# Kernel optimization log

Hardware: AMD Instinct MI355X
Metric: run time of the kernel (lower is better)

The kernel has to match this reference:

```python
import jax, jax.numpy as jnp
import numpy as np

HIDDEN = 2048
N_HEADS = 32
N_KV = 8
HEAD_DIM = HIDDEN // N_HEADS  # 64
GROUP = N_HEADS // N_KV       # 4
FFN = 8192
EPS = 1e-5
ROPE_BASE = 500000.0
NEG = -1e9


def rms_norm(x, w, eps=EPS):
    var = jnp.mean(x * x, axis=-1, keepdims=True)
    return x * jax.lax.rsqrt(var + eps) * w


def rope_cos_sin(position_ids):
    # inv_freq: [head_dim//2]
    inv_freq = 1.0 / (ROPE_BASE ** (jnp.arange(0, HEAD_DIM, 2, dtype=jnp.float32) / HEAD_DIM))
    freqs = position_ids.astype(jnp.float32)[:, :, None] * inv_freq[None, None, :]  # [b,s,d/2]
    emb = jnp.concatenate([freqs, freqs], axis=-1)  # [b,s,d]
    return jnp.cos(emb), jnp.sin(emb)


def rotate_half(x):
    x1, x2 = jnp.split(x, 2, axis=-1)
    return jnp.concatenate([-x2, x1], axis=-1)


def setup_inputs() -> dict:
    key = jax.random.key(0)
    ks = jax.random.split(key, 12)
    b, s = 2, 1024
    scale_h = 1.0 / np.sqrt(HIDDEN)
    scale_f = 1.0 / np.sqrt(FFN)
    hidden_states = jax.random.normal(ks[0], (b, s, HIDDEN), jnp.float32)
    causal = jnp.where(jnp.tril(jnp.ones((s, s), bool)), 0.0, NEG).astype(jnp.float32)
    attention_mask = jnp.broadcast_to(causal[None, None], (b, 1, s, s))
    position_ids = jnp.broadcast_to(jnp.arange(s, dtype=jnp.int32)[None], (b, s))
    return {
        "hidden_states": hidden_states,
        "attention_mask": attention_mask,
        "wq": jax.random.normal(ks[1], (HIDDEN, N_HEADS * HEAD_DIM), jnp.float32) * scale_h,
        "wk": jax.random.normal(ks[2], (HIDDEN, N_KV * HEAD_DIM), jnp.float32) * scale_h,
        "wv": jax.random.normal(ks[3], (HIDDEN, N_KV * HEAD_DIM), jnp.float32) * scale_h,
        "wo": jax.random.normal(ks[4], (N_HEADS * HEAD_DIM, HIDDEN), jnp.float32) * scale_h,
        "norm1_w": jnp.ones((HIDDEN,), jnp.float32),
        "norm2_w": jnp.ones((HIDDEN,), jnp.float32),
        "w_gate": jax.random.normal(ks[5], (HIDDEN, FFN), jnp.float32) * scale_h,
        "w_up": jax.random.normal(ks[6], (HIDDEN, FFN), jnp.float32) * scale_h,
        "w_down": jax.random.normal(ks[7], (FFN, HIDDEN), jnp.float32) * scale_f,
        "position_ids": position_ids,
    }


def reference(hidden_states, attention_mask, wq, wk, wv, wo, norm1_w, norm2_w,
              w_gate, w_up, w_down, position_ids):
    b, s, _ = hidden_states.shape
    residual = hidden_states
    normed = rms_norm(hidden_states, norm1_w)

    q = (normed @ wq).reshape(b, s, N_HEADS, HEAD_DIM).transpose(0, 2, 1, 3)  # [b,H,s,d]
    k = (normed @ wk).reshape(b, s, N_KV, HEAD_DIM).transpose(0, 2, 1, 3)    # [b,G,s,d]
    v = (normed @ wv).reshape(b, s, N_KV, HEAD_DIM).transpose(0, 2, 1, 3)

    cos, sin = rope_cos_sin(position_ids)  # [b,s,d]
    cos, sin = cos[:, None], sin[:, None]  # unsqueeze head dim
    q = q * cos + rotate_half(q) * sin
    k = k * cos + rotate_half(k) * sin

    # repeat_kv: [b,G,s,d] -> [b,H,s,d]
    k = jnp.repeat(k, GROUP, axis=1)
    v = jnp.repeat(v, GROUP, axis=1)

    scores = jnp.einsum('bhqd,bhkd->bhqk', q, k)
    scores = scores + attention_mask  # mask added BEFORE scaling, as in source
    attn = jax.nn.softmax(scores / np.sqrt(HEAD_DIM), axis=-1)
    ctx = jnp.einsum('bhqk,bhkd->bhqd', attn, v)
    ctx = ctx.transpose(0, 2, 1, 3).reshape(b, s, N_HEADS * HEAD_DIM)
    attn_out = ctx @ wo

    normed_ff = rms_norm(attn_out + residual, norm2_w)
    ff = (jax.nn.silu(normed_ff @ w_gate) * (normed_ff @ w_up)) @ w_down
    return attn_out + ff
```

## Files before the change

### kernel.cpp

```cpp
#include <hip/hip_runtime.h>
#include <hip/hip_bf16.h>
#include <cstddef>
#include <cstdint>

#define T_TOK   2048
#define HID     2048
#define NHEADS  32
#define NKV     8
#define HDIM    64
#define FFN_DIM 8192
#define QKV_N   3072

typedef __hip_bfloat16 bf16;
typedef __attribute__((ext_vector_type(8))) short short8;
typedef __attribute__((ext_vector_type(4))) float f32x4;
typedef __attribute__((ext_vector_type(4))) unsigned short us4;

typedef __attribute__((address_space(1))) const void cg_void;
typedef __attribute__((address_space(3))) void lds_void;

__global__ __launch_bounds__(256) void cast_transpose(const float* __restrict__ in,
                                                      bf16* __restrict__ out,
                                                      int K, int N)
{
    __shared__ bf16 t[64][65];
    const int n0 = blockIdx.x * 64, k0 = blockIdx.y * 64;
    const int tn = threadIdx.x & 63, tk = threadIdx.x >> 6;
    #pragma unroll
    for (int kk = tk; kk < 64; kk += 4)
        t[kk][tn] = __float2bfloat16(in[(size_t)(k0 + kk) * N + n0 + tn]);
    __syncthreads();
    #pragma unroll
    for (int nn = tk; nn < 64; nn += 4)
        out[(size_t)(n0 + nn) * K + k0 + tn] = t[tn][nn];
}

__global__ __launch_bounds__(256) void cast_ilv(const float* __restrict__ in,
                                                bf16* __restrict__ out,
                                                int N, int is_up)
{
    __shared__ bf16 t[64][65];
    const int n0 = blockIdx.x * 64, k0 = blockIdx.y * 64;
    const int tn = threadIdx.x & 63, tk = threadIdx.x >> 6;
    #pragma unroll
    for (int kk = tk; kk < 64; kk += 4)
        t[kk][tn] = __float2bfloat16(in[(size_t)(k0 + kk) * N + n0 + tn]);
    __syncthreads();
    #pragma unroll
    for (int nn = tk; nn < 64; nn += 4) {
        int n = n0 + nn;
        int r = ((n >> 5) << 6) + (is_up << 5) + (n & 31);
        out[(size_t)r * HID + k0 + tn] = t[tn][nn];
    }
}

__global__ __launch_bounds__(256) void rmsnorm_kernel(const float* __restrict__ x,
                                                      const float* __restrict__ w,
                                                      bf16* __restrict__ out)
{
    __shared__ float sm[4];
    const int row = blockIdx.x, tid = threadIdx.x;
    const float4* xr = (const float4*)(x + (size_t)row * HID);
    float4 a = xr[tid], b = xr[tid + 256];
    float ss = a.x*a.x + a.y*a.y + a.z*a.z + a.w*a.w
             + b.x*b.x + b.y*b.y + b.z*b.z + b.w*b.w;
    #pragma unroll
    for (int off = 32; off; off >>= 1) ss += __shfl_down(ss, off);
    if ((tid & 63) == 0) sm[tid >> 6] = ss;
    __syncthreads();
    float sc = rsqrtf((sm[0] + sm[1] + sm[2] + sm[3]) * (1.0f / HID) + 1e-5f);
    const float4* wr = (const float4*)w;
    float4 w0 = wr[tid], w1 = wr[tid + 256];
    bf16* o = out + (size_t)row * HID;
    o[tid*4+0] = __float2bfloat16(a.x * sc * w0.x);
    o[tid*4+1] = __float2bfloat16(a.y * sc * w0.y);
    o[tid*4+2] = __float2bfloat16(a.z * sc * w0.z);
    o[tid*4+3] = __float2bfloat16(a.w * sc * w0.w);
    o[1024+tid*4+0] = __float2bfloat16(b.x * sc * w1.x);
    o[1024+tid*4+1] = __float2bfloat16(b.y * sc * w1.y);
    o[1024+tid*4+2] = __float2bfloat16(b.z * sc * w1.z);
    o[1024+tid*4+3] = __float2bfloat16(b.w * sc * w1.w);
}

__global__ __launch_bounds__(256) void rmsnorm_add_kernel(const float* __restrict__ xa,
                                                          const float* __restrict__ xb,
                                                          const float* __restrict__ w,
                                                          bf16* __restrict__ out)
{
    __shared__ float sm[4];
    const int row = blockIdx.x, tid = threadIdx.x;
    const float4* ar = (const float4*)(xa + (size_t)row * HID);
    const float4* br = (const float4*)(xb + (size_t)row * HID);
    float4 a0 = ar[tid], a1 = ar[tid + 256];
    float4 b0 = br[tid], b1 = br[tid + 256];
    float4 s0, s1;
    s0.x = a0.x + b0.x; s0.y = a0.y + b0.y; s0.z = a0.z + b0.z; s0.w = a0.w + b0.w;
    s1.x = a1.x + b1.x; s1.y = a1.y + b1.y; s1.z = a1.z + b1.z; s1.w = a1.w + b1.w;
    float ss = s0.x*s0.x + s0.y*s0.y + s0.z*s0.z + s0.w*s0.w
             + s1.x*s1.x + s1.y*s1.y + s1.z*s1.z + s1.w*s1.w;
    #pragma unroll
    for (int off = 32; off; off >>= 1) ss += __shfl_down(ss, off);
    if ((tid & 63) == 0) sm[tid >> 6] = ss;
    __syncthreads();
    float sc = rsqrtf((sm[0] + sm[1] + sm[2] + sm[3]) * (1.0f / HID) + 1e-5f);
    const float4* wr = (const float4*)w;
    float4 w0 = wr[tid], w1 = wr[tid + 256];
    bf16* o = out + (size_t)row * HID;
    o[tid*4+0] = __float2bfloat16(s0.x * sc * w0.x);
    o[tid*4+1] = __float2bfloat16(s0.y * sc * w0.y);
    o[tid*4+2] = __float2bfloat16(s0.z * sc * w0.z);
    o[tid*4+3] = __float2bfloat16(s0.w * sc * w0.w);
    o[1024+tid*4+0] = __float2bfloat16(s1.x * sc * w1.x);
    o[1024+tid*4+1] = __float2bfloat16(s1.y * sc * w1.y);
    o[1024+tid*4+2] = __float2bfloat16(s1.z * sc * w1.z);
    o[1024+tid*4+3] = __float2bfloat16(s1.w * sc * w1.w);
}

template<int BN, int EPI>
__device__ __forceinline__ void gemm_body(
    const bf16* __restrict__ A, const bf16* __restrict__ Bt,
    float* __restrict__ Cf, bf16* __restrict__ Cb,
    int lda, int kbeg, int klen, int ldc, int bx, int by)
{
    constexpr int NFR = BN / 32;
    constexpr int BCH = BN / 32;
    __shared__ bf16 As[128 * 64];
    __shared__ bf16 Bs[BN * 64];
    const int tid = threadIdx.x;
    const int wv = tid >> 6, ln = tid & 63;
    const int wr = wv >> 1, wc = wv & 1;
    const size_t m0 = (size_t)by * 128;
    const size_t n0 = (size_t)bx * BN;

    const int lrow = ln >> 3;
    const int lk   = (ln & 7) ^ lrow;

    f32x4 acc[4][NFR] = {};

    const bf16* Abase = A  + (m0 + (size_t)wv*32 + lrow) * lda + kbeg + lk*8;
    const bf16* Bbase = Bt + (n0 + (size_t)wv*BCH*8 + lrow) * lda + kbeg + lk*8;
    bf16* AsW = As + wv*4*512;
    bf16* BsW = Bs + wv*BCH*512;

    for (int kt = 0; kt < klen; kt += 64) {
        #pragma unroll
        for (int i = 0; i < 4; ++i)
            __builtin_amdgcn_global_load_lds((cg_void*)(Abase + (size_t)i*8*lda + kt),
                                             (lds_void*)(AsW + i*512), 16, 0, 0);
        #pragma unroll
        for (int i = 0; i < BCH; ++i)
            __builtin_amdgcn_global_load_lds((cg_void*)(Bbase + (size_t)i*8*lda + kt),
                                             (lds_void*)(BsW + i*512), 16, 0, 0);
        __syncthreads();
        #pragma unroll
        for (int ks = 0; ks < 2; ++ks) {
            short8 af[4], bfg[NFR];
            const int kbyte = ks*64 + (ln >> 4)*16;
            #pragma unroll
            for (int m = 0; m < 4; ++m) {
                int row = wr*64 + m*16 + (ln & 15);
                af[m] = *(const short8*)((const char*)As + row*128 + (kbyte ^ ((row & 7) << 4)));
            }
            #pragma unroll
            for (int n = 0; n < NFR; ++n) {
                int row = wc*(BN/2) + n*16 + (ln & 15);
                bfg[n] = *(const short8*)((const char*)Bs + row*128 + (kbyte ^ ((row & 7) << 4)));
            }
            #pragma unroll
            for (int m = 0; m < 4; ++m)
                #pragma unroll
                for (int n = 0; n < NFR; ++n)
                    acc[m][n] = __builtin_amdgcn_mfma_f32_16x16x32_bf16(af[m], bfg[n], acc[m][n], 0, 0, 0);
        }
        __syncthreads();
    }

    const int cj = ln & 15, rj = ln >> 4;
    if constexpr (EPI == 4) {
        #pragma unroll
        for (int m = 0; m < 4; ++m) {
            #pragma unroll
            for (int j = 0; j < 4; ++j) {
                size_t row = m0 + wr*64 + m*16 + rj*4 + j;
                #pragma unroll
                for (int n = 0; n < 2; ++n) {
                    int col = ((int)(n0 >> 6) + wc) * 32 + n*16 + cj;
                    float g = acc[m][n][j];
                    float u = acc[m][n+2][j];
                    Cb[row * (size_t)ldc + col] =
                        __float2bfloat16(g / (1.0f + __expf(-g)) * u);
                }
            }
        }
    } else {
        #pragma unroll
        for (int m = 0; m < 4; ++m) {
            #pragma unroll
            for (int j = 0; j < 4; ++j) {
                size_t row = m0 + wr*64 + m*16 + rj*4 + j;
                #pragma unroll
                for (int n = 0; n < NFR; ++n) {
                    int col = (int)n0 + wc*(BN/2) + n*16 + cj;
                    float v = acc[m][n][j];
                    size_t off = row * (size_t)ldc + col;
                    if constexpr (EPI == 0) Cf[off] = v;
                    else if constexpr (EPI == 5) unsafeAtomicAdd(&Cf[off], v);
                }
            }
        }
    }
}

__device__ __forceinline__ void swz(int& bx, int& by) {
    const int nwg = gridDim.x * gridDim.y;
    int orig = blockIdx.y * gridDim.x + blockIdx.x;
    int wg = (orig & 7) * (nwg >> 3) + (orig >> 3);
    by = wg % gridDim.y;
    bx = wg / gridDim.y;
}

__global__ __launch_bounds__(256) void g_qkv(const bf16* __restrict__ A,
                                             const bf16* __restrict__ Bt,
                                             float* __restrict__ C) {
    int bx, by; swz(bx, by);
    gemm_body<64,0>(A, Bt, C, nullptr, HID, 0, HID, QKV_N, bx, by);
}
__global__ __launch_bounds__(256) void g_wo(const bf16* __restrict__ A,
                                            const bf16* __restrict__ Bt,
                                            float* __restrict__ C) {
    int bx, by; swz(bx, by);
    gemm_body<64,0>(A, Bt, C, nullptr, HID, 0, HID, HID, bx, by);
}
__global__ __launch_bounds__(256) void g_gateup(const bf16* __restrict__ A,
                                                const bf16* __restrict__ Bt,
                                                bf16* __restrict__ C) {
    int bx, by; swz(bx, by);
    gemm_body<128,4>(A, Bt, nullptr, C, HID, 0, HID, FFN_DIM, bx, by);
}
__global__ __launch_bounds__(256) void g_down(const bf16* __restrict__ A,
                                              const bf16* __restrict__ Bt,
                                              float* __restrict__ C) {
    int bx, by; swz(bx, by);
    gemm_body<64,5>(A, Bt, C, nullptr, FFN_DIM, blockIdx.z * 4096, 4096, HID, bx, by);
}

__global__ __launch_bounds__(256) void rope_cast(const float* __restrict__ qkv,
                                                 const int* __restrict__ pos_ids,
                                                 bf16* __restrict__ Qp,
                                                 bf16* __restrict__ Kp)
{
    const int t = blockIdx.x, tid = threadIdx.x;
    const int b = t >> 10, s = t & 1023;
    const float pos = (float)pos_ids[t];
    const float* row = qkv + (size_t)t * QKV_N;

    {
        int idx = tid * 4;
        int hq = idx >> 5, j = idx & 31;
        float xa[4], xb[4];
        *(float4*)xa = *(const float4*)(row + hq*64 + j);
        *(float4*)xb = *(const float4*)(row + hq*64 + j + 32);
        us4 o1, o2;
        #pragma unroll
        for (int jj = 0; jj < 4; ++jj) {
            float inv = exp2f(-(float)(j + jj) * 0.5916115177913804f);
            float ang = pos * inv, c, sn;
            sincosf(ang, &sn, &c);
            o1[jj] = __bfloat16_as_ushort(__float2bfloat16(xa[jj]*c - xb[jj]*sn));
            o2[jj] = __bfloat16_as_ushort(__float2bfloat16(xb[jj]*c + xa[jj]*sn));
        }
        bf16* qd = Qp + ((size_t)(b*32 + hq)*1024 + s)*64;
        *(us4*)(qd + j)      = o1;
        *(us4*)(qd + j + 32) = o2;
    }
    {
        int hk = tid >> 5, j = tid & 31;
        float a = row[2048 + hk*64 + j];
        float bb = row[2048 + hk*64 + j + 32];
        float inv = exp2f(-(float)j * 0.5916115177913804f);
        float ang = pos * inv, c, sn;
        sincosf(ang, &sn, &c);
        bf16* kd = Kp + ((size_t)(b*8 + hk)*1024 + s)*64;
        kd[j]      = __float2bfloat16(a*c - bb*sn);
        kd[j + 32] = __float2bfloat16(bb*c + a*sn);
    }
}

__global__ __launch_bounds__(256) void vt_cast(const float* __restrict__ qkv,
                                               bf16* __restrict__ Vt)
{
    __shared__ bf16 tile[64][64];
    const int s0 = blockIdx.x * 64;
    const int sec = blockIdx.y;
    const int b = sec >> 3, hk = sec & 7;
    const int tid = threadIdx.x;
    const float* base = qkv + ((size_t)(b*1024 + s0)) * QKV_N + 2560 + hk*64;
    const int srow = tid >> 2, d0 = (tid & 3) * 16;
    #pragma unroll
    for (int q = 0; q < 4; ++q) {
        float va[4];
        *(float4*)va = *(const float4*)(base + (size_t)srow * QKV_N + d0 + q*4);
        #pragma unroll
        for (int cc = 0; cc < 4; ++cc)
            tile[d0 + q*4 + cc][srow] = __float2bfloat16(va[cc]);
    }
    __syncthreads();
    const int dr = tid >> 2, sc = (tid & 3) * 16;
    bf16* od = Vt + ((size_t)sec*64 + dr)*1024 + s0 + sc;
    *(short8*)od       = *(const short8*)&tile[dr][sc];
    *(short8*)(od + 8) = *(const short8*)&tile[dr][sc + 8];
}

__global__ __launch_bounds__(256) void attn_mfma(const bf16* __restrict__ Qp,
                                                 const bf16* __restrict__ Kp,
                                                 const bf16* __restrict__ Vt,
                                                 bf16* __restrict__ ctx)
{
    __shared__ bf16 Ks[128 * 64];
    __shared__ bf16 Vs[64 * 128];
    __shared__ bf16 Ps[4 * 32 * 128];
    const int tid = threadIdx.x;
    const int w = tid >> 6, ln = tid & 63;
    const int qt = blockIdx.x, h = blockIdx.y, b = blockIdx.z;
    const int hk = h >> 2;
    const int q0 = qt * 128;

    const bf16* qsec = Qp + ((size_t)(b*32 + h)*1024 + q0 + w*32)*64;
    const bf16* ksec = Kp + ((size_t)(b*8 + hk)*1024)*64;
    const bf16* vsec = Vt + ((size_t)(b*8 + hk))*64*1024;

    short8 qf[2][2];
    #pragma unroll
    for (int f = 0; f < 2; ++f)
        #pragma unroll
        for (int kc = 0; kc < 2; ++kc)
            qf[f][kc] = *(const short8*)(qsec + (size_t)(f*16 + (ln & 15))*64 + kc*32 + (ln >> 4)*8);

    f32x4 acc_o[2][4] = {};
    f32x4 m[2], l[2];
    #pragma unroll
    for (int f = 0; f < 2; ++f)
        #pragma unroll
        for (int j = 0; j < 4; ++j) { m[f][j] = -1e30f; l[f][j] = 0.0f; }

    const int lrow = ln >> 3;
    const int lkk  = (ln & 7) ^ lrow;
    char* PsW = (char*)Ps + w * 8192;

    const int ntiles = qt + 1;
    for (int kt = 0; kt < ntiles; ++kt) {
        const int kv0 = kt * 128;
        {
            const bf16* kbase = ksec + (size_t)(kv0 + w*32 + lrow)*64 + lkk*8;
            bf16* KsW = Ks + w*2048;
            #pragma unroll
            for (int i = 0; i < 4; ++i)
                __builtin_amdgcn_global_load_lds((cg_void*)(kbase + (size_t)i*8*64),
                                                 (lds_void*)(KsW + i*512), 16, 0, 0);
        }
        {
            bf16* VsW = Vs + w*2048;
            #pragma unroll
            for (int i = 0; i < 4; ++i) {
                int d = w*16 + i*4 + (ln >> 4);
                __builtin_amdgcn_global_load_lds(
                    (cg_void*)(vsec + (size_t)d*1024 + kv0 + (((ln & 15) ^ (d & 7))*8)),
                    (lds_void*)(VsW + i*512), 16, 0, 0);
            }
        }
        __syncthreads();

        f32x4 acc_s[2][8] = {};
        #pragma unroll
        for (int c = 0; c < 8; ++c) {
            int kvr = c*16 + (ln & 15);
            const char* krow = (const char*)Ks + kvr*128;
            short8 kf0 = *(const short8*)(krow + (((ln >> 4)*16)      ^ ((kvr & 7) << 4)));
            short8 kf1 = *(const short8*)(krow + ((64 + (ln >> 4)*16) ^ ((kvr & 7) << 4)));
            #pragma unroll
            for (int f = 0; f < 2; ++f) {
                acc_s[f][c] = __builtin_amdgcn_mfma_f32_16x16x32_bf16(qf[f][0], kf0, acc_s[f][c], 0, 0, 0);
                acc_s[f][c] = __builtin_amdgcn_mfma_f32_16x16x32_bf16(qf[f][1], kf1, acc_s[f][c], 0, 0, 0);
            }
        }

        const bool diag = (kt == qt);
        f32x4 vmax[2];
        #pragma unroll
        for (int f = 0; f < 2; ++f)
            #pragma unroll
            for (int j = 0; j < 4; ++j) vmax[f][j] = -1e30f;
        #pragma unroll
        for (int f = 0; f < 2; ++f) {
            #pragma unroll
            for (int c = 0; c < 8; ++c) {
                f32x4 t = acc_s[f][c] * 0.125f;
                if (diag) {
                    int kv = kv0 + c*16 + (ln & 15);
                    int qg = q0 + w*32 + f*16 + (ln >> 4)*4;
                    #pragma unroll
                    for (int j = 0; j < 4; ++j)
                        if (kv > qg + j) t[j] = -1e30f;
                }
                acc_s[f][c] = t;
                #pragma unroll
                for (int j = 0; j < 4; ++j) vmax[f][j] = fmaxf(vmax[f][j], t[j]);
            }
            #pragma unroll
            for (int mk = 1; mk <= 8; mk <<= 1)
                #pragma unroll
                for (int j = 0; j < 4; ++j)
                    vmax[f][j] = fmaxf(vmax[f][j], __shfl_xor(vmax[f][j], mk));
        }

        #pragma unroll
        for (int f = 0; f < 2; ++f) {
            f32x4 r;
            #pragma unroll
            for (int j = 0; j < 4; ++j) {
                float mn = fmaxf(m[f][j], vmax[f][j]);
                r[j] = __expf(m[f][j] - mn);
                m[f][j] = mn;
                l[f][j] *= r[j];
            }
            #pragma unroll
            for (int df = 0; df < 4; ++df)
                #pragma unroll
                for (int j = 0; j < 4; ++j) acc_o[f][df][j] *= r[j];
        }

        f32x4 rs[2] = {};
        #pragma unroll
        for (int f = 0; f < 2; ++f) {
            #pragma unroll
            for (int c = 0; c < 8; ++c) {
                #pragma unroll
                for (int j = 0; j < 4; ++j) {
                    float p = __expf(acc_s[f][c][j] - m[f][j]);
                    rs[f][j] += p;
                    int qloc = f*16 + (ln >> 4)*4 + j;
                    int kvb  = (c*16 + (ln & 15))*2;
                    *(bf16*)(PsW + qloc*256 + (kvb ^ ((qloc & 7) << 4))) = __float2bfloat16(p);
                }
            }
            #pragma unroll
            for (int mk = 1; mk <= 8; mk <<= 1)
                #pragma unroll
                for (int j = 0; j < 4; ++j)
                    rs[f][j] += __shfl_xor(rs[f][j], mk);
            #pragma unroll
            for (int j = 0; j < 4; ++j) l[f][j] += rs[f][j];
        }

        #pragma unroll
        for (int kc = 0; kc < 4; ++kc) {
            short8 pa[2];
            #pragma unroll
            for (int f = 0; f < 2; ++f) {
                int qloc = f*16 + (ln & 15);
                pa[f] = *(const short8*)(PsW + qloc*256 + ((kc*64 + (ln >> 4)*16) ^ ((qloc & 7) << 4)));
            }
            #pragma unroll
            for (int df = 0; df < 4; ++df) {
                int dl = df*16 + (ln & 15);
                short8 vfr = *(const short8*)((const char*)Vs + dl*256 + ((kc*64 + (ln >> 4)*16) ^ ((dl & 7) << 4)));
                #pragma unroll
                for (int f = 0; f < 2; ++f)
                    acc_o[f][df] = __builtin_amdgcn_mfma_f32_16x16x32_bf16(pa[f], vfr, acc_o[f][df], 0, 0, 0);
            }
        }
        __syncthreads();
    }

    #pragma unroll
    for (int f = 0; f < 2; ++f) {
        f32x4 inv;
        #pragma unroll
        for (int j = 0; j < 4; ++j) inv[j] = 1.0f / l[f][j];
        #pragma unroll
        for (int df = 0; df < 4; ++df) {
            #pragma unroll
            for (int j = 0; j < 4; ++j) {
                int q = q0 + w*32 + f*16 + (ln >> 4)*4 + j;
                int d = df*16 + (ln & 15);
                ctx[((size_t)b*1024 + q)*HID + h*64 + d] = __float2bfloat16(acc_o[f][df][j] * inv[j]);
            }
        }
    }
}

extern "C" void kernel_launch(void* const* d_in, const int* in_sizes, int n_in,
                              void* d_out, int out_size, void* d_ws, size_t ws_size,
                              hipStream_t stream)
{
    const float* hidden = (const float*)d_in[0];
    const float* wq = (const float*)d_in[2];
    const float* wk = (const float*)d_in[3];
    const float* wv = (const float*)d_in[4];
    const float* wo = (const float*)d_in[5];
    const float* n1 = (const float*)d_in[6];
    const float* n2 = (const float*)d_in[7];
    const float* wg = (const float*)d_in[8];
    const float* wu = (const float*)d_in[9];
    const float* wd = (const float*)d_in[10];
    const int*  pos = (const int*)d_in[11];
    float* out = (float*)d_out;
    char* ws = (char*)d_ws;

    bf16* wgu_t  = (bf16*)(ws + 0);
    bf16* wd_t   = (bf16*)(ws + 67108864);
    bf16* wqkv_t = (bf16*)(ws + 100663296);
    bf16* wo_t   = (bf16*)(ws + 113246208);
    bf16* normed = (bf16*)(ws + 121634816);
    float* qkv   = (float*)(ws + 130023424);
    bf16* ctx    = (bf16*)(ws + 155189248);
    bf16* hb     = (bf16*)(ws + 130023424);
    bf16* Qp     = (bf16*)(ws + 121634816);
    bf16* Kp     = (bf16*)(ws + 163577856);
    bf16* Vt     = (bf16*)(ws + 165675008);

    cast_transpose<<<dim3(32, 32), 256, 0, stream>>>(wq, wqkv_t, 2048, 2048);
    cast_transpose<<<dim3(8, 32),  256, 0, stream>>>(wk, wqkv_t + 4194304, 2048, 512);
    cast_transpose<<<dim3(8, 32),  256, 0, stream>>>(wv, wqkv_t + 5242880, 2048, 512);
    cast_transpose<<<dim3(32, 32), 256, 0, stream>>>(wo, wo_t, 2048, 2048);
    cast_ilv<<<dim3(128, 32), 256, 0, stream>>>(wg, wgu_t, FFN_DIM, 0);
    cast_ilv<<<dim3(128, 32), 256, 0, stream>>>(wu, wgu_t, FFN_DIM, 1);
    cast_transpose<<<dim3(32, 128),256, 0, stream>>>(wd, wd_t, 8192, 2048);

    rmsnorm_kernel<<<T_TOK, 256, 0, stream>>>(hidden, n1, normed);
    g_qkv<<<dim3(QKV_N/64, T_TOK/128), 256, 0, stream>>>(normed, wqkv_t, qkv);
    rope_cast<<<T_TOK, 256, 0, stream>>>(qkv, pos, Qp, Kp);
    vt_cast<<<dim3(16, 16), 256, 0, stream>>>(qkv, Vt);
    attn_mfma<<<dim3(8, NHEADS, 2), 256, 0, stream>>>(Qp, Kp, Vt, ctx);
    g_wo<<<dim3(HID/64, T_TOK/128), 256, 0, stream>>>(ctx, wo_t, out);
    rmsnorm_add_kernel<<<T_TOK, 256, 0, stream>>>(out, hidden, n2, normed);
    g_gateup<<<dim3(16384/128, T_TOK/128), 256, 0, stream>>>(normed, wgu_t, hb);
    g_down<<<dim3(HID/64, T_TOK/128, 2), 256, 0, stream>>>(hb, wd_t, out);
}
```

Measured before the change: 556.1 us.

## Double-buffer GEMM LDS tiles with async prefetch two stages ahead

Converts the shared GEMM body from a single-buffered load-sync-compute loop to a two-stage LDS ring. The next K tile is loaded via global_load_lds while MFMAs run on the current one. Fragments are read into registers before the barrier, then the buffer is refilled, and manual vmcnt/lgkmcnt waits with s_setprio are meant to hide global memory latency. This doubles LDS use per block, which may reduce occupancy, and relies on hand-placed wait counts being correct.

```diff
diff --git a/kernel.cpp b/kernel.cpp
--- a/kernel.cpp
+++ b/kernel.cpp
@@ -122,10 +122,10 @@
     float* __restrict__ Cf, bf16* __restrict__ Cb,
     int lda, int kbeg, int klen, int ldc, int bx, int by)
 {
-    constexpr int NFR = BN / 32;
-    constexpr int BCH = BN / 32;
-    __shared__ bf16 As[128 * 64];
-    __shared__ bf16 Bs[BN * 64];
+    constexpr int NFR   = BN / 32;
+    constexpr int CALLS = 4 + NFR;
+    __shared__ bf16 As[2 * 128 * 64];
+    __shared__ bf16 Bs[2 * BN * 64];
     const int tid = threadIdx.x;
     const int wv = tid >> 6, ln = tid & 63;
     const int wr = wv >> 1, wc = wv & 1;
@@ -135,44 +135,73 @@
     const int lrow = ln >> 3;
     const int lk   = (ln & 7) ^ lrow;
 
+    const bf16* Abase = A  + (m0 + (size_t)wv*32 + lrow) * lda + kbeg + lk*8;
+    const bf16* Bbase = Bt + (n0 + (size_t)wv*NFR*8 + lrow) * lda + kbeg + lk*8;
+    bf16* AsW = As + wv*2048;
+    bf16* BsW = Bs + wv*NFR*512;
+
+    auto stage = [&](int p, int tk) {
+        #pragma unroll
+        for (int i = 0; i < 4; ++i)
+            __builtin_amdgcn_global_load_lds((cg_void*)(Abase + (size_t)i*8*lda + tk),
+                                             (lds_void*)(AsW + p*8192 + i*512), 16, 0, 0);
+        #pragma unroll
+        for (int i = 0; i < NFR; ++i)
+            __builtin_amdgcn_global_load_lds((cg_void*)(Bbase + (size_t)i*8*lda + tk),
+                                             (lds_void*)(BsW + p*(BN*64) + i*512), 16, 0, 0);
+    };
+
     f32x4 acc[4][NFR] = {};
-
-    const bf16* Abase = A  + (m0 + (size_t)wv*32 + lrow) * lda + kbeg + lk*8;
-    const bf16* Bbase = Bt + (n0 + (size_t)wv*BCH*8 + lrow) * lda + kbeg + lk*8;
-    bf16* AsW = As + wv*4*512;
-    bf16* BsW = Bs + wv*BCH*512;
-
-    for (int kt = 0; kt < klen; kt += 64) {
-        #pragma unroll
-        for (int i = 0; i < 4; ++i)
-            __builtin_amdgcn_global_load_lds((cg_void*)(Abase + (size_t)i*8*lda + kt),
-                                             (lds_void*)(AsW + i*512), 16, 0, 0);
-        #pragma unroll
-        for (int i = 0; i < BCH; ++i)
-            __builtin_amdgcn_global_load_lds((cg_void*)(Bbase + (size_t)i*8*lda + kt),
-                                             (lds_void*)(BsW + i*512), 16, 0, 0);
-        __syncthreads();
+    const int nt = klen >> 6;
+
+    stage(0, 0);
+    stage(1, 64);
+    asm volatile("s_waitcnt vmcnt(%0)" :: "n"(CALLS) : "memory");
+    __builtin_amdgcn_sched_barrier(0);
+    __builtin_amdgcn_s_barrier();
+
+    for (int t = 0; t < nt; ++t) {
+        const int p = t & 1;
+        const char* Ab = (const char*)As + p * 16384;
+        const char* Bb = (const char*)Bs + p * (BN * 128);
+
+        short8 af[4][2], bfr[NFR][2];
         #pragma unroll
         for (int ks = 0; ks < 2; ++ks) {
-            short8 af[4], bfg[NFR];
             const int kbyte = ks*64 + (ln >> 4)*16;
             #pragma unroll
             for (int m = 0; m < 4; ++m) {
                 int row = wr*64 + m*16 + (ln & 15);
-                af[m] = *(const short8*)((const char*)As + row*128 + (kbyte ^ ((row & 7) << 4)));
+                af[m][ks] = *(const short8*)(Ab + row*128 + (kbyte ^ ((row & 7) << 4)));
             }
             #pragma unroll
             for (int n = 0; n < NFR; ++n) {
                 int row = wc*(BN/2) + n*16 + (ln & 15);
-                bfg[n] = *(const short8*)((const char*)Bs + row*128 + (kbyte ^ ((row & 7) << 4)));
-            }
+                bfr[n][ks] = *(const short8*)(Bb + row*128 + (kbyte ^ ((row & 7) << 4)));
+            }
+        }
+        asm volatile("s_waitcnt lgkmcnt(0)" ::: "memory");
+        __builtin_amdgcn_sched_barrier(0);
+        __builtin_amdgcn_s_barrier();
+
+        const bool more = (t + 2 < nt);
+        if (more) stage(p, (t + 2) * 64);
+        __builtin_amdgcn_sched_barrier(0);
+
+        __builtin_amdgcn_s_setprio(1);
+        #pragma unroll
+        for (int ks = 0; ks < 2; ++ks)
             #pragma unroll
             for (int m = 0; m < 4; ++m)
                 #pragma unroll
                 for (int n = 0; n < NFR; ++n)
-                    acc[m][n] = __builtin_amdgcn_mfma_f32_16x16x32_bf16(af[m], bfg[n], acc[m][n], 0, 0, 0);
-        }
-        __syncthreads();
+                    acc[m][n] = __builtin_amdgcn_mfma_f32_16x16x32_bf16(af[m][ks], bfr[n][ks], acc[m][n], 0, 0, 0);
+        __builtin_amdgcn_s_setprio(0);
+
+        if (more) { asm volatile("s_waitcnt vmcnt(%0)" :: "n"(CALLS) : "memory"); }
+        else      { asm volatile("s_waitcnt vmcnt(0)" ::: "memory"); }
+        __builtin_amdgcn_sched_barrier(0);
+        __builtin_amdgcn_s_barrier();
     }
 
     const int cj = ln & 15, rj = ln >> 4;
```

Result: faster. 539.9 us (-2.9%).
